# Kernel optimization log

Measured on AMD Instinct MI355X. Metric: run time of the kernel, lower is better.

## Reference

```python
import jax, jax.numpy as jnp
import numpy as np

N, E, F, H, C = 100000, 1600000, 128, 128, 40
NUM_LAYERS = 4
BN_EPS = 1e-5


def gcn_conv(x, src, dst, W, b, n):
    # PyG GCNConv with improved=True: self-loop edge weight 2.0
    e = src.shape[0]
    deg = jax.ops.segment_sum(jnp.ones((e,), x.dtype), dst, num_segments=n) + 2.0
    dinv = jnp.where(deg > 0, jax.lax.rsqrt(deg), 0.0)  # [n]
    xw = x @ W  # [n, out]
    coef = dinv[src] * dinv[dst]  # [e]
    agg = jax.ops.segment_sum(xw[src] * coef[:, None], dst, num_segments=n)
    agg = agg + (2.0 * dinv * dinv)[:, None] * xw  # self-loop term (weight 2)
    return agg + b


def batchnorm(x, gamma, beta):
    # training-mode BN (batch statistics, biased variance), eps=1e-5
    mu = jnp.mean(x, axis=0)
    var = jnp.mean(jnp.square(x - mu), axis=0)
    return (x - mu) * jax.lax.rsqrt(var + BN_EPS) * gamma + beta


def setup_inputs() -> dict:
    key = jax.random.key(0)
    ks = jax.random.split(key, 4)
    x = jax.random.normal(ks[0], (N, F), dtype=jnp.float32)
    edge_index = jax.random.randint(ks[1], (2, E), 0, N, dtype=jnp.int32)
    conv_w = jax.random.normal(ks[2], (NUM_LAYERS, F, H), dtype=jnp.float32) * 0.05
    conv_b = jnp.zeros((NUM_LAYERS, H), jnp.float32)
    bn_g = jnp.ones((NUM_LAYERS, H), jnp.float32)
    bn_b = jnp.zeros((NUM_LAYERS, H), jnp.float32)
    fc_w = jax.random.normal(ks[3], (NUM_LAYERS + 1, H, C), dtype=jnp.float32) * 0.05
    fc_b = jnp.zeros((NUM_LAYERS + 1, C), jnp.float32)
    return {"x": x, "edge_index": edge_index, "conv_w": conv_w, "conv_b": conv_b,
            "bn_g": bn_g, "bn_b": bn_b, "fc_w": fc_w, "fc_b": fc_b}


def reference(x, edge_index, conv_w, conv_b, bn_g, bn_b, fc_w, fc_b):
    n = x.shape[0]
    src, dst = edge_index[0], edge_index[1]
    outs = [x]
    h = x
    for i in range(NUM_LAYERS):
        h = gcn_conv(h, src, dst, conv_w[i], conv_b[i], n)
        h = batchnorm(h, bn_g[i], bn_b[i])
        h = jax.nn.relu(h)
        outs.append(h)
    # jumping-knowledge style sum of per-layer class heads (dropout = identity in eval)
    out = outs[0] @ fc_w[0] + fc_b[0]
    for i in range(1, NUM_LAYERS + 1):
        out = out + outs[i] @ fc_w[i] + fc_b[i]
    return jax.nn.log_softmax(out, axis=-1)
```

## Files before the change

### kernel.cpp

```cpp
#include <hip/hip_runtime.h>
#include <hip/hip_bf16.h>
#include <stdint.h>

#define NN 100000
#define NE 1600000
#define FD 128
#define CD 40
#define NL 4
#define NTB 391
#define TILE 4096
#define NTILES 391
#define EBCAP 8192
#define OCAP 5120

typedef __bf16 bf16;
typedef __bf16 bf16x8 __attribute__((ext_vector_type(8)));
typedef float f32x4 __attribute__((ext_vector_type(4)));

__device__ __forceinline__ unsigned short f2b(float f) {
  bf16 b = (bf16)f;
  unsigned short u;
  __builtin_memcpy(&u, &b, 2);
  return u;
}
__device__ __forceinline__ float lo16(unsigned int u) { return __uint_as_float(u << 16); }
__device__ __forceinline__ float hi16(unsigned int u) { return __uint_as_float(u & 0xffff0000u); }

__launch_bounds__(256)
__global__ void k_bfill(const int* __restrict__ src, const int* __restrict__ dst,
                        int* __restrict__ gcur, unsigned int* __restrict__ csrE) {
  __shared__ int cnt[NTB], pref[NTB], gofs[NTB];
  __shared__ int sc[512];
  __shared__ unsigned int stage[TILE];
  __shared__ unsigned short tgtb[TILE];
  int tid = threadIdx.x;
  int base = blockIdx.x * TILE;
  int tcnt = min(TILE, NE - base);
  for (int b = tid; b < NTB; b += 256) cnt[b] = 0;
  __syncthreads();
  unsigned int pay[16];
  int brk[16];
#pragma unroll
  for (int i = 0; i < 16; i++) {
    int e = base + tid + i * 256;
    if (e < NE) {
      int d = dst[e];
      int b = d >> 8;
      int r = atomicAdd(&cnt[b], 1);
      pay[i] = (unsigned int)src[e] | ((unsigned int)(d & 255) << 17);
      brk[i] = (b << 12) | r;
    } else {
      brk[i] = -1;
    }
  }
  __syncthreads();
  sc[tid] = (tid < NTB) ? cnt[tid] : 0;
  sc[tid + 256] = (tid + 256 < NTB) ? cnt[tid + 256] : 0;
  __syncthreads();
  for (int off = 1; off < 512; off <<= 1) {
    int a0 = (tid >= off) ? sc[tid - off] : 0;
    int a1 = sc[tid + 256 - off];
    __syncthreads();
    sc[tid] += a0;
    sc[tid + 256] += a1;
    __syncthreads();
  }
  for (int b = tid; b < NTB; b += 256) pref[b] = sc[b] - cnt[b];
  __syncthreads();
#pragma unroll
  for (int i = 0; i < 16; i++) {
    if (brk[i] >= 0) {
      int b = brk[i] >> 12, r = brk[i] & 4095;
      int p = pref[b] + r;
      if ((unsigned)p < (unsigned)TILE) {
        stage[p] = pay[i];
        tgtb[p] = (unsigned short)b;
      }
    }
  }
  for (int b = tid; b < NTB; b += 256) {
    int c = cnt[b];
    gofs[b] = c ? atomicAdd(&gcur[b], (c + 15) & ~15) : 0;
  }
  __syncthreads();
  for (int t = tid; t < tcnt; t += 256) {
    int b = tgtb[t];
    int pos = gofs[b] + (t - pref[b]);
    if ((unsigned)pos < (unsigned)EBCAP) csrE[(size_t)b * EBCAP + pos] = stage[t];
  }
  for (int b = tid; b < NTB; b += 256) {
    int c = cnt[b];
    if (c) {
      int pad = (c + 15) & ~15;
      for (int j = c; j < pad; j++) {
        int pos = gofs[b] + j;
        if ((unsigned)pos < (unsigned)EBCAP) csrE[(size_t)b * EBCAP + pos] = 0xFFFFFFFFu;
      }
    }
  }
}

__launch_bounds__(256)
__global__ void k_bsort(const int* __restrict__ gcur, const unsigned int* __restrict__ csrE,
                        unsigned int* __restrict__ csrp, float* __restrict__ dinv,
                        int2* __restrict__ rse) {
  __shared__ unsigned int ent[OCAP];
  __shared__ int c32[256], prefn[256], c2[256], sc[256];
  __shared__ int ecnt_s;
  int b = blockIdx.x, tid = threadIdx.x;
  c32[tid] = 0;
  c2[tid] = 0;
  if (tid == 0) ecnt_s = 0;
  __syncthreads();
  int claimed = min(gcur[b], EBCAP);
  const unsigned int* in = csrE + (size_t)b * EBCAP;
  for (int i = tid; i < claimed; i += 256) {
    unsigned int e = in[i];
    if (e != 0xFFFFFFFFu) {
      int idx = atomicAdd(&ecnt_s, 1);
      if (idx < OCAP) ent[idx] = e;
      atomicAdd(&c32[e >> 17], 1);
    }
  }
  __syncthreads();
  int cnt = min(ecnt_s, OCAP);
  int c = c32[tid];
  int pc = (c + 3) & ~3;
  sc[tid] = pc;
  __syncthreads();
  for (int off = 1; off < 256; off <<= 1) {
    int a = (tid >= off) ? sc[tid - off] : 0;
    __syncthreads();
    sc[tid] += a;
    __syncthreads();
  }
  prefn[tid] = sc[tid] - pc;
  int node = b * 256 + tid;
  if (node < NN) {
    dinv[node] = rsqrtf((float)c + 2.0f);
    int s = b * OCAP + prefn[tid];
    rse[node] = make_int2(s, s + pc);
  }
  for (int j = c; j < pc; j++) {
    int pos = prefn[tid] + j;
    if (pos < OCAP) csrp[b * OCAP + pos] = 0x1FFFFu;
  }
  __syncthreads();
  for (int i = tid; i < cnt; i += 256) {
    unsigned int e = ent[i];
    int dlo = e >> 17;
    int ofs = atomicAdd(&c2[dlo], 1);
    int pos = prefn[dlo] + ofs;
    if (pos < OCAP) csrp[b * OCAP + pos] = e & 0x1FFFFu;
  }
}

__global__ void k_pack(unsigned int* __restrict__ csrp, const float* __restrict__ dinv) {
  int i = blockIdx.x * 256 + threadIdx.x;
  unsigned int e = csrp[i];
  unsigned int s = e & 0x1FFFFu;
  unsigned int fix = 0;
  if (s < NN) {
    fix = (unsigned int)__float2uint_rn(dinv[s] * 32768.0f);
  } else {
    s = 0;
  }
  csrp[i] = (fix << 17) | s;
}

__global__ void k_repackall(const float* __restrict__ wc, const float* __restrict__ wf,
                            bf16* __restrict__ wp, bf16* __restrict__ wpfc) {
  int t = blockIdx.x * 256 + threadIdx.x;
  if (t < NL * 16384) {
    int j = t & 7, lane = (t >> 3) & 63, n0 = (t >> 9) & 7, k0 = (t >> 12) & 3, layer = t >> 14;
    int k = k0 * 32 + (lane >> 4) * 8 + j;
    int n = n0 * 16 + (lane & 15);
    wp[t] = (bf16)wc[(layer * 128 + k) * 128 + n];
    return;
  }
  t -= NL * 16384;
  if (t >= 5 * 6144) return;
  int j = t & 7, lane = (t >> 3) & 63;
  int rest = t >> 9;
  int n0 = rest % 3;
  int rest2 = rest / 3;
  int k0 = rest2 & 3, layer = rest2 >> 2;
  int k = k0 * 32 + (lane >> 4) * 8 + j;
  int n = n0 * 16 + (lane & 15);
  wpfc[t] = (n < CD) ? (bf16)wf[(layer * 128 + k) * CD + n] : (bf16)0.0f;
}

template <int NC, bool BN, bool INIT, bool LSM>
__launch_bounds__(256)
__global__ void k_gfc(const void* __restrict__ inp, const float* __restrict__ stats,
                      const float* __restrict__ g, const float* __restrict__ bb,
                      const bf16* __restrict__ wconv, const bf16* __restrict__ wfc,
                      const float* __restrict__ fcb, bf16* __restrict__ xwb,
                      float* __restrict__ out) {
  __shared__ bf16 wl[NC * 2048 + 6144];
  __shared__ float sc[128], sh[128];
  int tid = threadIdx.x;
  if (NC) {
    const uint4* gc = (const uint4*)wconv;
    uint4* lc = (uint4*)wl;
#pragma unroll
    for (int i = 0; i < NC; i++) lc[tid + i * 256] = gc[tid + i * 256];
  }
  {
    const uint4* gf = (const uint4*)wfc;
    uint4* lf = (uint4*)(wl + NC * 2048);
    for (int i = tid; i < 768; i += 256) lf[i] = gf[i];
  }
  if (BN && tid < 128) {
    const float invN = 1.0f / (float)NN;
    float s1 = stats[tid] + stats[256 + tid] + stats[512 + tid] + stats[768 + tid];
    float s2 = stats[128 + tid] + stats[384 + tid] + stats[640 + tid] + stats[896 + tid];
    float mu = s1 * invN;
    float var = s2 * invN - mu * mu;
    float s = g[tid] * rsqrtf(var + 1e-5f);
    sc[tid] = s;
    sh[tid] = bb[tid] - mu * s;
  }
  __syncthreads();
  int wid = tid >> 6, lane = tid & 63, quad = lane >> 4, l15 = lane & 15;
  int m_base = blockIdx.x * 64 + wid * 16;
  int arow = m_base + l15;
  if (arow >= NN) arow = NN - 1;
  f32x4 accc[NC > 0 ? NC : 1];
  f32x4 accf[3];
  if (NC) {
#pragma unroll
    for (int i = 0; i < NC; i++) accc[i] = (f32x4){0.f, 0.f, 0.f, 0.f};
  }
#pragma unroll
  for (int i = 0; i < 3; i++) accf[i] = (f32x4){0.f, 0.f, 0.f, 0.f};
#pragma unroll
  for (int k0 = 0; k0 < 4; k0++) {
    union Fr { bf16x8 v; unsigned short us[8]; } fr;
    if (BN) {
      const uint4* prow = (const uint4*)((const bf16*)inp + (size_t)arow * 128 + k0 * 32 + quad * 8);
      uint4 u = *prow;
      unsigned int uu[4] = {u.x, u.y, u.z, u.w};
      int kc = k0 * 32 + quad * 8;
#pragma unroll
      for (int p = 0; p < 4; p++) {
        float x0 = lo16(uu[p]) * sc[kc + 2 * p] + sh[kc + 2 * p];
        float x1 = hi16(uu[p]) * sc[kc + 2 * p + 1] + sh[kc + 2 * p + 1];
        fr.us[2 * p] = f2b(fmaxf(0.f, x0));
        fr.us[2 * p + 1] = f2b(fmaxf(0.f, x1));
      }
    } else {
      const float* prow = (const float*)inp + (size_t)arow * 128 + k0 * 32 + quad * 8;
      float4 u0 = *(const float4*)prow;
      float4 u1 = *(const float4*)(prow + 4);
      fr.us[0] = f2b(u0.x); fr.us[1] = f2b(u0.y); fr.us[2] = f2b(u0.z); fr.us[3] = f2b(u0.w);
      fr.us[4] = f2b(u1.x); fr.us[5] = f2b(u1.y); fr.us[6] = f2b(u1.z); fr.us[7] = f2b(u1.w);
    }
    bf16x8 a = fr.v;
    if (NC) {
#pragma unroll
      for (int n0 = 0; n0 < NC; n0++) {
        bf16x8 bfr = *reinterpret_cast<const bf16x8*>(&wl[(k0 * NC + n0) * 512 + lane * 8]);
        accc[n0] = __builtin_amdgcn_mfma_f32_16x16x32_bf16(a, bfr, accc[n0], 0, 0, 0);
      }
    }
#pragma unroll
    for (int n0 = 0; n0 < 3; n0++) {
      bf16x8 bfr = *reinterpret_cast<const bf16x8*>(&wl[NC * 2048 + (k0 * 3 + n0) * 512 + lane * 8]);
      accf[n0] = __builtin_amdgcn_mfma_f32_16x16x32_bf16(a, bfr, accf[n0], 0, 0, 0);
    }
  }
  int orow = m_base + quad * 4;
  if (NC) {
#pragma unroll
    for (int n0 = 0; n0 < NC; n0++) {
#pragma unroll
      for (int r2 = 0; r2 < 4; r2++) {
        int row = orow + r2;
        if (row < NN) xwb[(size_t)row * 128 + n0 * 16 + l15] = (bf16)accc[n0][r2];
      }
    }
  }
  if (!LSM) {
#pragma unroll
    for (int n0 = 0; n0 < 3; n0++) {
      int col = n0 * 16 + l15;
      if (col < CD) {
        float bias = fcb[col];
#pragma unroll
        for (int r2 = 0; r2 < 4; r2++) {
          int row = orow + r2;
          if (row < NN) {
            size_t idx = (size_t)row * CD + col;
            float v = accf[n0][r2] + bias;
            out[idx] = INIT ? v : out[idx] + v;
          }
        }
      }
    }
  } else {
    float bias[3];
#pragma unroll
    for (int n0 = 0; n0 < 3; n0++) {
      int col = n0 * 16 + l15;
      bias[n0] = (col < CD) ? fcb[col] : 0.f;
    }
#pragma unroll
    for (int r2 = 0; r2 < 4; r2++) {
      int row = orow + r2;
      float v[3];
#pragma unroll
      for (int n0 = 0; n0 < 3; n0++) {
        int col = n0 * 16 + l15;
        if (col < CD) {
          float prev = (row < NN) ? out[(size_t)row * CD + col] : 0.f;
          v[n0] = prev + accf[n0][r2] + bias[n0];
        } else {
          v[n0] = -1e30f;
        }
      }
      float m = fmaxf(v[0], fmaxf(v[1], v[2]));
#pragma unroll
      for (int s = 1; s < 16; s <<= 1) m = fmaxf(m, __shfl_xor(m, s, 64));
      float sum = 0.f;
#pragma unroll
      for (int n0 = 0; n0 < 3; n0++) {
        int col = n0 * 16 + l15;
        if (col < CD) sum += __expf(v[n0] - m);
      }
#pragma unroll
      for (int s = 1; s < 16; s <<= 1) sum += __shfl_xor(sum, s, 64);
      float ls = m + logf(sum);
      if (row < NN) {
#pragma unroll
        for (int n0 = 0; n0 < 3; n0++) {
          int col = n0 * 16 + l15;
          if (col < CD) out[(size_t)row * CD + col] = v[n0] - ls;
        }
      }
    }
  }
}

__launch_bounds__(256)
__global__ void k_gather(const uint4* __restrict__ xw, const int2* __restrict__ rse,
                         const unsigned int* __restrict__ csrp, const float* __restrict__ dinv,
                         uint4* __restrict__ aggb) {
  int tid = threadIdx.x;
  int n = blockIdx.x * 4 + (tid >> 6);
  int l = tid & 63;
  int h = l >> 4, cl = l & 15;
  float dn = dinv[n];
  float kk = dn * (1.0f / 32768.0f);
  uint4 u = xw[n * 16 + cl];
  float cs = (h == 0) ? 2.0f * dn * dn : 0.0f;
  float a0 = cs * lo16(u.x), a1 = cs * hi16(u.x);
  float a2 = cs * lo16(u.y), a3 = cs * hi16(u.y);
  float a4 = cs * lo16(u.z), a5 = cs * hi16(u.z);
  float a6 = cs * lo16(u.w), a7 = cs * hi16(u.w);
  int2 r = rse[n];
  int e = r.x, e1 = r.y;
  for (; e + 7 < e1; e += 8) {
    unsigned int p0 = csrp[e + h];
    unsigned int p1 = csrp[e + 4 + h];
    uint4 v0 = xw[(p0 & 0x1FFFFu) * 16 + cl];
    uint4 v1 = xw[(p1 & 0x1FFFFu) * 16 + cl];
    float c0 = (float)(p0 >> 17) * kk;
    float c1 = (float)(p1 >> 17) * kk;
    a0 += c0 * lo16(v0.x); a1 += c0 * hi16(v0.x);
    a2 += c0 * lo16(v0.y); a3 += c0 * hi16(v0.y);
    a4 += c0 * lo16(v0.z); a5 += c0 * hi16(v0.z);
    a6 += c0 * lo16(v0.w); a7 += c0 * hi16(v0.w);
    a0 += c1 * lo16(v1.x); a1 += c1 * hi16(v1.x);
    a2 += c1 * lo16(v1.y); a3 += c1 * hi16(v1.y);
    a4 += c1 * lo16(v1.z); a5 += c1 * hi16(v1.z);
    a6 += c1 * lo16(v1.w); a7 += c1 * hi16(v1.w);
  }
  if (e < e1) {
    unsigned int p0 = csrp[e + h];
    uint4 v0 = xw[(p0 & 0x1FFFFu) * 16 + cl];
    float c0 = (float)(p0 >> 17) * kk;
    a0 += c0 * lo16(v0.x); a1 += c0 * hi16(v0.x);
    a2 += c0 * lo16(v0.y); a3 += c0 * hi16(v0.y);
    a4 += c0 * lo16(v0.z); a5 += c0 * hi16(v0.z);
    a6 += c0 * lo16(v0.w); a7 += c0 * hi16(v0.w);
  }
  a0 += __shfl_xor(a0, 16, 64); a0 += __shfl_xor(a0, 32, 64);
  a1 += __shfl_xor(a1, 16, 64); a1 += __shfl_xor(a1, 32, 64);
  a2 += __shfl_xor(a2, 16, 64); a2 += __shfl_xor(a2, 32, 64);
  a3 += __shfl_xor(a3, 16, 64); a3 += __shfl_xor(a3, 32, 64);
  a4 += __shfl_xor(a4, 16, 64); a4 += __shfl_xor(a4, 32, 64);
  a5 += __shfl_xor(a5, 16, 64); a5 += __shfl_xor(a5, 32, 64);
  a6 += __shfl_xor(a6, 16, 64); a6 += __shfl_xor(a6, 32, 64);
  a7 += __shfl_xor(a7, 16, 64); a7 += __shfl_xor(a7, 32, 64);
  if (h == 0) {
    uint4 o;
    o.x = (unsigned int)f2b(a0) | ((unsigned int)f2b(a1) << 16);
    o.y = (unsigned int)f2b(a2) | ((unsigned int)f2b(a3) << 16);
    o.z = (unsigned int)f2b(a4) | ((unsigned int)f2b(a5) << 16);
    o.w = (unsigned int)f2b(a6) | ((unsigned int)f2b(a7) << 16);
    aggb[n * 16 + cl] = o;
  }
}

__launch_bounds__(256)
__global__ void k_stats(const uint2* __restrict__ agg, float* __restrict__ statsL) {
  __shared__ float ls1[128], ls2[128];
  int tid = threadIdx.x;
  if (tid < 128) { ls1[tid] = 0.f; ls2[tid] = 0.f; }
  __syncthreads();
  int cl = tid & 31, rg = tid >> 5;
  float s10 = 0.f, s11 = 0.f, s12 = 0.f, s13 = 0.f;
  float s20 = 0.f, s21 = 0.f, s22 = 0.f, s23 = 0.f;
  for (int r = blockIdx.x * 8 + rg; r < NN; r += 2048) {
    uint2 u = agg[r * 32 + cl];
    float b0 = lo16(u.x), b1 = hi16(u.x), b2 = lo16(u.y), b3 = hi16(u.y);
    s10 += b0; s20 += b0 * b0;
    s11 += b1; s21 += b1 * b1;
    s12 += b2; s22 += b2 * b2;
    s13 += b3; s23 += b3 * b3;
  }
  atomicAdd(&ls1[4 * cl + 0], s10);
  atomicAdd(&ls1[4 * cl + 1], s11);
  atomicAdd(&ls1[4 * cl + 2], s12);
  atomicAdd(&ls1[4 * cl + 3], s13);
  atomicAdd(&ls2[4 * cl + 0], s20);
  atomicAdd(&ls2[4 * cl + 1], s21);
  atomicAdd(&ls2[4 * cl + 2], s22);
  atomicAdd(&ls2[4 * cl + 3], s23);
  __syncthreads();
  if (tid < 128) {
    float* st = statsL + (blockIdx.x & 3) * 256;
    atomicAdd(&st[tid], ls1[tid]);
    atomicAdd(&st[128 + tid], ls2[tid]);
  }
}

static inline size_t alup(size_t x) { return (x + 255) & ~(size_t)255; }

extern "C" void kernel_launch(void* const* d_in, const int* in_sizes, int n_in,
                              void* d_out, int out_size, void* d_ws, size_t ws_size,
                              hipStream_t stream) {
  char* p = (char*)d_ws;
  bf16* xwb = (bf16*)p;     p += alup((size_t)NN * FD * 2);
  bf16* aggb = (bf16*)p;    p += alup((size_t)NN * FD * 2);
  float* dinv = (float*)p;  p += alup((size_t)NN * 4);
  int2* rse = (int2*)p;     p += alup((size_t)NN * 8);
  int* gcur = (int*)p;      p += alup((size_t)NTB * 4);
  unsigned int* csrE = (unsigned int*)p; p += alup((size_t)NTB * EBCAP * 4);
  unsigned int* csrp = (unsigned int*)p; p += alup((size_t)NTB * OCAP * 4);
  bf16* wp = (bf16*)p;      p += alup((size_t)NL * 16384 * 2);
  bf16* wpfc = (bf16*)p;    p += alup((size_t)5 * 6144 * 2);
  float* stats = (float*)p; p += alup((size_t)NL * 1024 * 4);

  const float* x = (const float*)d_in[0];
  const int* ei = (const int*)d_in[1];
  const int* srcv = ei;
  const int* dstv = ei + NE;
  const float* convw = (const float*)d_in[2];
  const float* bng = (const float*)d_in[4];
  const float* bnb = (const float*)d_in[5];
  const float* fcw = (const float*)d_in[6];
  const float* fcb = (const float*)d_in[7];
  float* out = (float*)d_out;

  hipMemsetAsync(gcur, 0, (size_t)NTB * sizeof(int), stream);
  hipMemsetAsync(stats, 0, (size_t)NL * 1024 * sizeof(float), stream);
  k_bfill<<<NTILES, 256, 0, stream>>>(srcv, dstv, gcur, csrE);
  k_bsort<<<NTB, 256, 0, stream>>>(gcur, csrE, csrp, dinv, rse);
  k_pack<<<NTB * OCAP / 256, 256, 0, stream>>>(csrp, dinv);
  k_repackall<<<(NL * 16384 + 5 * 6144 + 255) / 256, 256, 0, stream>>>(convw, fcw, wp, wpfc);

  k_gfc<8, false, true, false><<<1563, 256, 0, stream>>>(x, nullptr, nullptr, nullptr,
                                                         wp, wpfc, fcb, xwb, out);

  for (int L = 0; L < NL; L++) {
    k_gather<<<NN / 4, 256, 0, stream>>>((const uint4*)xwb, rse, csrp, dinv,
                                         (uint4*)aggb);
    float* st = stats + (size_t)L * 1024;
    k_stats<<<256, 256, 0, stream>>>((const uint2*)aggb, st);
    if (L < NL - 1) {
      k_gfc<8, true, false, false><<<1563, 256, 0, stream>>>(aggb, st, bng + L * FD, bnb + L * FD,
                                                             wp + (size_t)(L + 1) * 16384,
                                                             wpfc + (size_t)(L + 1) * 6144,
                                                             fcb + (L + 1) * CD, xwb, out);
    } else {
      k_gfc<0, true, false, true><<<1563, 256, 0, stream>>>(aggb, st, bng + L * FD, bnb + L * FD,
                                                            nullptr,
                                                            wpfc + (size_t)(L + 1) * 6144,
                                                            fcb + (L + 1) * CD, nullptr, out);
    }
  }
}
```

Before: 588.9 us.

## Fuse BN stats into gather, merge setup kernels, widen stats replicas

Batch-norm statistics are now accumulated inside the gather kernel from the fp32 sums before bf16 rounding, which removes the separate stats pass that re-read the aggregated activations each layer. Per-block partials go to 64 replicated stat slots to reduce global atomic contention, and the consumer sums all 64 replicas. Weight repacking is merged into the bucket-fill launch as extra blocks, CSR packing is merged into the first GEMM launch as extra blocks, and the two memsets become one. The cost is many more shared-memory atomics per node in the gather kernel and slightly different numerics, since stats now come from unrounded values.

```diff
diff --git a/kernel.cpp b/kernel.cpp
--- a/kernel.cpp
+++ b/kernel.cpp
@@ -12,6 +12,10 @@
 #define NTILES 391
 #define EBCAP 8192
 #define OCAP 5120
+#define NREP 64
+#define RPB 376
+#define PKB 512
+#define GFCB 1563
 
 typedef __bf16 bf16;
 typedef __bf16 bf16x8 __attribute__((ext_vector_type(8)));
@@ -28,12 +32,36 @@
 
 __launch_bounds__(256)
 __global__ void k_bfill(const int* __restrict__ src, const int* __restrict__ dst,
-                        int* __restrict__ gcur, unsigned int* __restrict__ csrE) {
+                        int* __restrict__ gcur, unsigned int* __restrict__ csrE,
+                        const float* __restrict__ wc, const float* __restrict__ wf,
+                        bf16* __restrict__ wp, bf16* __restrict__ wpfc) {
   __shared__ int cnt[NTB], pref[NTB], gofs[NTB];
   __shared__ int sc[512];
   __shared__ unsigned int stage[TILE];
   __shared__ unsigned short tgtb[TILE];
   int tid = threadIdx.x;
+  if (blockIdx.x >= NTILES) {
+    int t = (blockIdx.x - NTILES) * 256 + tid;
+    if (t < NL * 16384) {
+      int j = t & 7, lane = (t >> 3) & 63, n0 = (t >> 9) & 7, k0 = (t >> 12) & 3, layer = t >> 14;
+      int k = k0 * 32 + (lane >> 4) * 8 + j;
+      int n = n0 * 16 + (lane & 15);
+      wp[t] = (bf16)wc[(layer * 128 + k) * 128 + n];
+    } else {
+      t -= NL * 16384;
+      if (t < 5 * 6144) {
+        int j = t & 7, lane = (t >> 3) & 63;
+        int rest = t >> 9;
+        int n0 = rest % 3;
+        int rest2 = rest / 3;
+        int k0 = rest2 & 3, layer = rest2 >> 2;
+        int k = k0 * 32 + (lane >> 4) * 8 + j;
+        int n = n0 * 16 + (lane & 15);
+        wpfc[t] = (n < CD) ? (bf16)wf[(layer * 128 + k) * CD + n] : (bf16)0.0f;
+      }
+    }
+    return;
+  }
   int base = blockIdx.x * TILE;
   int tcnt = min(TILE, NE - base);
   for (int b = tid; b < NTB; b += 256) cnt[b] = 0;
@@ -155,51 +183,31 @@
   }
 }
 
-__global__ void k_pack(unsigned int* __restrict__ csrp, const float* __restrict__ dinv) {
-  int i = blockIdx.x * 256 + threadIdx.x;
-  unsigned int e = csrp[i];
-  unsigned int s = e & 0x1FFFFu;
-  unsigned int fix = 0;
-  if (s < NN) {
-    fix = (unsigned int)__float2uint_rn(dinv[s] * 32768.0f);
-  } else {
-    s = 0;
-  }
-  csrp[i] = (fix << 17) | s;
-}
-
-__global__ void k_repackall(const float* __restrict__ wc, const float* __restrict__ wf,
-                            bf16* __restrict__ wp, bf16* __restrict__ wpfc) {
-  int t = blockIdx.x * 256 + threadIdx.x;
-  if (t < NL * 16384) {
-    int j = t & 7, lane = (t >> 3) & 63, n0 = (t >> 9) & 7, k0 = (t >> 12) & 3, layer = t >> 14;
-    int k = k0 * 32 + (lane >> 4) * 8 + j;
-    int n = n0 * 16 + (lane & 15);
-    wp[t] = (bf16)wc[(layer * 128 + k) * 128 + n];
-    return;
-  }
-  t -= NL * 16384;
-  if (t >= 5 * 6144) return;
-  int j = t & 7, lane = (t >> 3) & 63;
-  int rest = t >> 9;
-  int n0 = rest % 3;
-  int rest2 = rest / 3;
-  int k0 = rest2 & 3, layer = rest2 >> 2;
-  int k = k0 * 32 + (lane >> 4) * 8 + j;
-  int n = n0 * 16 + (lane & 15);
-  wpfc[t] = (n < CD) ? (bf16)wf[(layer * 128 + k) * CD + n] : (bf16)0.0f;
-}
-
-template <int NC, bool BN, bool INIT, bool LSM>
+template <int NC, bool BN, bool INIT, bool LSM, bool PACK>
 __launch_bounds__(256)
 __global__ void k_gfc(const void* __restrict__ inp, const float* __restrict__ stats,
                       const float* __restrict__ g, const float* __restrict__ bb,
                       const bf16* __restrict__ wconv, const bf16* __restrict__ wfc,
                       const float* __restrict__ fcb, bf16* __restrict__ xwb,
-                      float* __restrict__ out) {
+                      float* __restrict__ out,
+                      unsigned int* __restrict__ csrp, const float* __restrict__ dinvp) {
   __shared__ bf16 wl[NC * 2048 + 6144];
   __shared__ float sc[128], sh[128];
   int tid = threadIdx.x;
+  if (PACK && blockIdx.x >= GFCB) {
+    for (int i = (blockIdx.x - GFCB) * 256 + tid; i < NTB * OCAP; i += PKB * 256) {
+      unsigned int e = csrp[i];
+      unsigned int s = e & 0x1FFFFu;
+      unsigned int fix = 0;
+      if (s < NN) {
+        fix = (unsigned int)__float2uint_rn(dinvp[s] * 32768.0f);
+      } else {
+        s = 0;
+      }
+      csrp[i] = (fix << 17) | s;
+    }
+    return;
+  }
   if (NC) {
     const uint4* gc = (const uint4*)wconv;
     uint4* lc = (uint4*)wl;
@@ -213,8 +221,12 @@
   }
   if (BN && tid < 128) {
     const float invN = 1.0f / (float)NN;
-    float s1 = stats[tid] + stats[256 + tid] + stats[512 + tid] + stats[768 + tid];
-    float s2 = stats[128 + tid] + stats[384 + tid] + stats[640 + tid] + stats[896 + tid];
+    float s1 = 0.f, s2 = 0.f;
+#pragma unroll 8
+    for (int r = 0; r < NREP; r++) {
+      s1 += stats[r * 256 + tid];
+      s2 += stats[r * 256 + 128 + tid];
+    }
     float mu = s1 * invN;
     float var = s2 * invN - mu * mu;
     float s = g[tid] * rsqrtf(var + 1e-5f);
@@ -345,8 +357,11 @@
 __launch_bounds__(256)
 __global__ void k_gather(const uint4* __restrict__ xw, const int2* __restrict__ rse,
                          const unsigned int* __restrict__ csrp, const float* __restrict__ dinv,
-                         uint4* __restrict__ aggb) {
+                         uint4* __restrict__ aggb, float* __restrict__ statsL) {
+  __shared__ float ls1[128], ls2[128];
   int tid = threadIdx.x;
+  if (tid < 128) { ls1[tid] = 0.f; ls2[tid] = 0.f; }
+  __syncthreads();
   int n = blockIdx.x * 4 + (tid >> 6);
   int l = tid & 63;
   int h = l >> 4, cl = l & 15;
@@ -400,37 +415,19 @@
     o.z = (unsigned int)f2b(a4) | ((unsigned int)f2b(a5) << 16);
     o.w = (unsigned int)f2b(a6) | ((unsigned int)f2b(a7) << 16);
     aggb[n * 16 + cl] = o;
-  }
-}
-
-__launch_bounds__(256)
-__global__ void k_stats(const uint2* __restrict__ agg, float* __restrict__ statsL) {
-  __shared__ float ls1[128], ls2[128];
-  int tid = threadIdx.x;
-  if (tid < 128) { ls1[tid] = 0.f; ls2[tid] = 0.f; }
-  __syncthreads();
-  int cl = tid & 31, rg = tid >> 5;
-  float s10 = 0.f, s11 = 0.f, s12 = 0.f, s13 = 0.f;
-  float s20 = 0.f, s21 = 0.f, s22 = 0.f, s23 = 0.f;
-  for (int r = blockIdx.x * 8 + rg; r < NN; r += 2048) {
-    uint2 u = agg[r * 32 + cl];
-    float b0 = lo16(u.x), b1 = hi16(u.x), b2 = lo16(u.y), b3 = hi16(u.y);
-    s10 += b0; s20 += b0 * b0;
-    s11 += b1; s21 += b1 * b1;
-    s12 += b2; s22 += b2 * b2;
-    s13 += b3; s23 += b3 * b3;
-  }
-  atomicAdd(&ls1[4 * cl + 0], s10);
-  atomicAdd(&ls1[4 * cl + 1], s11);
-  atomicAdd(&ls1[4 * cl + 2], s12);
-  atomicAdd(&ls1[4 * cl + 3], s13);
-  atomicAdd(&ls2[4 * cl + 0], s20);
-  atomicAdd(&ls2[4 * cl + 1], s21);
-  atomicAdd(&ls2[4 * cl + 2], s22);
-  atomicAdd(&ls2[4 * cl + 3], s23);
+    int cb = cl * 8;
+    atomicAdd(&ls1[cb + 0], a0); atomicAdd(&ls2[cb + 0], a0 * a0);
+    atomicAdd(&ls1[cb + 1], a1); atomicAdd(&ls2[cb + 1], a1 * a1);
+    atomicAdd(&ls1[cb + 2], a2); atomicAdd(&ls2[cb + 2], a2 * a2);
+    atomicAdd(&ls1[cb + 3], a3); atomicAdd(&ls2[cb + 3], a3 * a3);
+    atomicAdd(&ls1[cb + 4], a4); atomicAdd(&ls2[cb + 4], a4 * a4);
+    atomicAdd(&ls1[cb + 5], a5); atomicAdd(&ls2[cb + 5], a5 * a5);
+    atomicAdd(&ls1[cb + 6], a6); atomicAdd(&ls2[cb + 6], a6 * a6);
+    atomicAdd(&ls1[cb + 7], a7); atomicAdd(&ls2[cb + 7], a7 * a7);
+  }
   __syncthreads();
   if (tid < 128) {
-    float* st = statsL + (blockIdx.x & 3) * 256;
+    float* st = statsL + (blockIdx.x & (NREP - 1)) * 256;
     atomicAdd(&st[tid], ls1[tid]);
     atomicAdd(&st[128 + tid], ls2[tid]);
   }
@@ -447,11 +444,11 @@
   float* dinv = (float*)p;  p += alup((size_t)NN * 4);
   int2* rse = (int2*)p;     p += alup((size_t)NN * 8);
   int* gcur = (int*)p;      p += alup((size_t)NTB * 4);
+  float* stats = (float*)p; p += alup((size_t)NL * NREP * 256 * 4);
   unsigned int* csrE = (unsigned int*)p; p += alup((size_t)NTB * EBCAP * 4);
   unsigned int* csrp = (unsigned int*)p; p += alup((size_t)NTB * OCAP * 4);
   bf16* wp = (bf16*)p;      p += alup((size_t)NL * 16384 * 2);
   bf16* wpfc = (bf16*)p;    p += alup((size_t)5 * 6144 * 2);
-  float* stats = (float*)p; p += alup((size_t)NL * 1024 * 4);
 
   const float* x = (const float*)d_in[0];
   const int* ei = (const int*)d_in[1];
@@ -464,31 +461,26 @@
   const float* fcb = (const float*)d_in[7];
   float* out = (float*)d_out;
 
-  hipMemsetAsync(gcur, 0, (size_t)NTB * sizeof(int), stream);
-  hipMemsetAsync(stats, 0, (size_t)NL * 1024 * sizeof(float), stream);
-  k_bfill<<<NTILES, 256, 0, stream>>>(srcv, dstv, gcur, csrE);
+  hipMemsetAsync(gcur, 0, alup((size_t)NTB * 4) + alup((size_t)NL * NREP * 256 * 4), stream);
+  k_bfill<<<NTILES + RPB, 256, 0, stream>>>(srcv, dstv, gcur, csrE, convw, fcw, wp, wpfc);
   k_bsort<<<NTB, 256, 0, stream>>>(gcur, csrE, csrp, dinv, rse);
-  k_pack<<<NTB * OCAP / 256, 256, 0, stream>>>(csrp, dinv);
-  k_repackall<<<(NL * 16384 + 5 * 6144 + 255) / 256, 256, 0, stream>>>(convw, fcw, wp, wpfc);
-
-  k_gfc<8, false, true, false><<<1563, 256, 0, stream>>>(x, nullptr, nullptr, nullptr,
-                                                         wp, wpfc, fcb, xwb, out);
+  k_gfc<8, false, true, false, true><<<GFCB + PKB, 256, 0, stream>>>(
+      x, nullptr, nullptr, nullptr, wp, wpfc, fcb, xwb, out, csrp, dinv);
 
   for (int L = 0; L < NL; L++) {
+    float* st = stats + (size_t)L * NREP * 256;
     k_gather<<<NN / 4, 256, 0, stream>>>((const uint4*)xwb, rse, csrp, dinv,
-                                         (uint4*)aggb);
-    float* st = stats + (size_t)L * 1024;
-    k_stats<<<256, 256, 0, stream>>>((const uint2*)aggb, st);
+                                         (uint4*)aggb, st);
     if (L < NL - 1) {
-      k_gfc<8, true, false, false><<<1563, 256, 0, stream>>>(aggb, st, bng + L * FD, bnb + L * FD,
-                                                             wp + (size_t)(L + 1) * 16384,
-                                                             wpfc + (size_t)(L + 1) * 6144,
-                                                             fcb + (L + 1) * CD, xwb, out);
+      k_gfc<8, true, false, false, false><<<GFCB, 256, 0, stream>>>(
+          aggb, st, bng + L * FD, bnb + L * FD,
+          wp + (size_t)(L + 1) * 16384, wpfc + (size_t)(L + 1) * 6144,
+          fcb + (L + 1) * CD, xwb, out, nullptr, nullptr);
     } else {
-      k_gfc<0, true, false, true><<<1563, 256, 0, stream>>>(aggb, st, bng + L * FD, bnb + L * FD,
-                                                            nullptr,
-                                                            wpfc + (size_t)(L + 1) * 6144,
-                                                            fcb + (L + 1) * CD, nullptr, out);
-    }
-  }
-}
+      k_gfc<0, true, false, true, false><<<GFCB, 256, 0, stream>>>(
+          aggb, st, bng + L * FD, bnb + L * FD,
+          nullptr, wpfc + (size_t)(L + 1) * 6144,
+          fcb + (L + 1) * CD, nullptr, out, nullptr, nullptr);
+    }
+  }
+}
```

Measured after the change: 936.3 us. 1.59x slower.
